# Performance work log

Measured on AMD Instinct MI355X. Metric: run time of the kernel, lower is better.

## Reference

```python
import jax, jax.numpy as jnp
import numpy as np

T, B, D_IN, H = 512, 256, 512, 128

def setup_inputs() -> dict:
    key = jax.random.key(0)
    ks = jax.random.split(key, 6)
    c0 = jax.random.normal(ks[0], (B, H), jnp.float32)
    h0 = jax.random.normal(ks[1], (B, H), jnp.float32)
    obs = jax.random.normal(ks[2], (T, B, D_IN), jnp.float32)
    done = jax.random.randint(ks[3], (T, B), 0, 2).astype(jnp.bool_)
    Wi = jax.random.normal(ks[4], (D_IN, 4 * H), jnp.float32) * (1.0 / np.sqrt(D_IN))
    Wh = jax.random.normal(ks[5], (H, 4 * H), jnp.float32) * (1.0 / np.sqrt(H))
    b = jnp.zeros((4 * H,), jnp.float32)
    return {"c0": c0, "h0": h0, "obs": obs, "done": done, "Wi": Wi, "Wh": Wh, "b": b}

def reference(c0, h0, obs, done, Wi, Wh, b):
    # Time-scanned flax LSTMCell with done-masked state reset.
    # Carry reset: where(done, initialize_carry()=zeros, old_state).
    # Flax LSTMCell gates (order i,f,g,o): sigmoid/sigmoid/tanh/sigmoid,
    # dense_i has no bias, dense_h has bias b.
    def step(carry, inp):
        c, h = carry
        x, d = inp                      # x: [B, D_IN], d: [B]
        keep = jnp.logical_not(d)[:, None]
        c = jnp.where(keep, c, 0.0)
        h = jnp.where(keep, h, 0.0)
        gates = x @ Wi + h @ Wh + b     # [B, 4H]
        i, f, g, o = jnp.split(gates, 4, axis=-1)
        new_c = jax.nn.sigmoid(f) * c + jax.nn.sigmoid(i) * jnp.tanh(g)
        new_h = jax.nn.sigmoid(o) * jnp.tanh(new_c)
        return (new_c, new_h), new_h

    (cT, hT), ys = jax.lax.scan(step, (c0, h0), (obs, done))
    return ys, cT, hT
```

## Files before the change

### kernel.cpp

```cpp
#include <hip/hip_runtime.h>
#include <hip/hip_bf16.h>
#include <cstdint>
#include <cstddef>

#define TT  512
#define BB  256
#define DIN 512
#define HH  128
#define NG  512

typedef __bf16 bf16x8 __attribute__((ext_vector_type(8)));
typedef float  f32x4  __attribute__((ext_vector_type(4)));

__device__ __forceinline__ float fast_sig(float x) {
  float e = __builtin_amdgcn_exp2f(-1.44269504f * x);
  return __builtin_amdgcn_rcpf(1.f + e);
}
__device__ __forceinline__ float fast_tanh(float x) {
  float e = __builtin_amdgcn_exp2f(-2.88539008f * x);
  return __builtin_fmaf(2.f, __builtin_amdgcn_rcpf(1.f + e), -1.f);
}

__device__ __forceinline__ void lgkm_barrier() {
  asm volatile("s_waitcnt lgkmcnt(0)\n\ts_barrier" ::: "memory");
}

__device__ __forceinline__ int ld_flag(const int* p) {
  return __hip_atomic_load(p, __ATOMIC_RELAXED, __HIP_MEMORY_SCOPE_AGENT);
}
__device__ __forceinline__ uint2 ld_xg8(const __bf16* p) {
  unsigned long long v = __hip_atomic_load((const unsigned long long*)p,
                                           __ATOMIC_RELAXED, __HIP_MEMORY_SCOPE_AGENT);
  union { unsigned long long u; uint2 v2; } cv; cv.u = v;
  return cv.v2;
}

__global__ void wconv_kernel(const float* __restrict__ Wi, const float* __restrict__ Wh,
                             __bf16* __restrict__ WiT, __bf16* __restrict__ WhT,
                             int* __restrict__ flags) {
  int idx = blockIdx.x * 256 + threadIdx.x;
  if (blockIdx.x == 0) {
    flags[threadIdx.x] = 0;
    flags[threadIdx.x + 256] = 0;
  }
  if (idx < DIN * NG) {
    int n = idx >> 9, k = idx & 511;
    WiT[(size_t)n * DIN + k] = (__bf16)Wi[(size_t)k * NG + n];
  }
  if (idx < HH * NG) {
    int n = idx >> 7, k = idx & 127;
    WhT[(size_t)n * HH + k] = (__bf16)Wh[(size_t)k * NG + n];
  }
}

__device__ __forceinline__ void gemm_body(
    const float* __restrict__ obs, const __bf16* __restrict__ WiT,
    const float* __restrict__ bias, __bf16* __restrict__ Xg,
    int* __restrict__ flags, int bid, __bf16 (*Alds)[40]) {
  const int tid  = threadIdx.x;
  const int wave = tid >> 6, lane = tid & 63;
  const int l15  = lane & 15, q = lane >> 4;
  const size_t m0 = (size_t)bid * 128;

  const f32x4 fzero = {0.f, 0.f, 0.f, 0.f};
  f32x4 acc[8][4];
#pragma unroll
  for (int i = 0; i < 8; i++)
#pragma unroll
    for (int jj = 0; jj < 4; jj++) acc[i][jj] = fzero;

  const int am = tid >> 2, aq = tid & 3;
  const float* aptr = obs + (m0 + am) * DIN + aq * 8;
  const __bf16* bptr[4];
#pragma unroll
  for (int nt = 0; nt < 4; nt++)
    bptr[nt] = WiT + (size_t)(wave * 64 + nt * 16 + l15) * DIN + q * 8;

  float4 a0[2], a1[2];
  bf16x8 bs[2][4];
  a0[0] = *(const float4*)(aptr);      a1[0] = *(const float4*)(aptr + 4);
  a0[1] = *(const float4*)(aptr + 32); a1[1] = *(const float4*)(aptr + 36);
#pragma unroll
  for (int nt = 0; nt < 4; nt++) {
    bs[0][nt] = *(const bf16x8*)(bptr[nt]);
    bs[1][nt] = *(const bf16x8*)(bptr[nt] + 32);
  }

#pragma unroll
  for (int kc = 0; kc < DIN; kc += 32) {
    const int sl = (kc >> 5) & 1;
    if (kc) lgkm_barrier();
    {
      float4 f0 = a0[sl], f1 = a1[sl];
      bf16x8 v = {(__bf16)f0.x, (__bf16)f0.y, (__bf16)f0.z, (__bf16)f0.w,
                  (__bf16)f1.x, (__bf16)f1.y, (__bf16)f1.z, (__bf16)f1.w};
      *(bf16x8*)&Alds[am][aq * 8] = v;
    }
    lgkm_barrier();
    int kp = kc + 64; if (kp > DIN - 32) kp = DIN - 32;
    a0[sl] = *(const float4*)(aptr + kp);
    a1[sl] = *(const float4*)(aptr + kp + 4);
#pragma unroll
    for (int mt = 0; mt < 8; mt++) {
      bf16x8 af = *(const bf16x8*)&Alds[mt * 16 + l15][q * 8];
#pragma unroll
      for (int nt = 0; nt < 4; nt++)
        acc[mt][nt] = __builtin_amdgcn_mfma_f32_16x16x32_bf16(af, bs[sl][nt], acc[mt][nt], 0, 0, 0);
    }
#pragma unroll
    for (int nt = 0; nt < 4; nt++)
      bs[sl][nt] = *(const bf16x8*)(bptr[nt] + kp);
  }

  const int t = bid >> 1;
  const int half = bid & 1;
#pragma unroll
  for (int mt = 0; mt < 8; mt++) {
    const int bg = half * 8 + mt;
#pragma unroll
    for (int nt = 0; nt < 4; nt++) {
      const int n = wave * 64 + nt * 16 + l15;
      const int g = n >> 7, jj = n & 127;
      const float bb = bias[n];
      __bf16* base = Xg + (size_t)(t * 16 + bg) * 4 * 2048 + jj * 16 + q * 4 + g;
#pragma unroll
      for (int r = 0; r < 4; r++)
        base[(size_t)r * 2048] = (__bf16)(acc[mt][nt][r] + bb);
    }
  }

  __syncthreads();
  if (tid == 0) {
    __threadfence();
    __hip_atomic_fetch_add(flags + t, 1, __ATOMIC_RELEASE, __HIP_MEMORY_SCOPE_AGENT);
  }
}

template<int R0>
__device__ __forceinline__ void scan_body(
    const __bf16* __restrict__ Xg, const __bf16* __restrict__ WhT,
    const int* __restrict__ done, const float* __restrict__ c0,
    const float* __restrict__ h0, float* __restrict__ out,
    const int* __restrict__ flags,
    int bg, __bf16 (*hlds)[16][HH + 8]) {
  const int tid  = threadIdx.x;
  const int wave = tid >> 6, lane = tid & 63;
  const int l15  = lane & 15, q = lane >> 4;
  const int b0 = bg * 16;
  const int j  = wave * 16 + l15;
  const int b  = b0 + q * 4 + R0;
  const int row = q * 4 + R0;

  bf16x8 bfrag[4][4];
#pragma unroll
  for (int g = 0; g < 4; g++)
#pragma unroll
    for (int ks = 0; ks < 4; ks++)
      bfrag[g][ks] = *(const bf16x8*)(WhT + (size_t)(g * HH + j) * HH + ks * 32 + q * 8);

  for (int i = tid; i < 2 * 16 * (HH + 8); i += 512) ((__bf16*)hlds)[i] = (__bf16)0.f;
  __syncthreads();
  const int d0 = done[b];
  float c = c0[(size_t)b * HH + j];
  hlds[0][row][j] = d0 ? (__bf16)0.f : (__bf16)h0[(size_t)b * HH + j];
  __syncthreads();

  const size_t tstride = (size_t)16 * 4 * 2048;
  const __bf16* xpA = Xg + (size_t)(bg * 4 + R0) * 2048 + j * 16 + q * 4;
  const __bf16* xpB = xpA + tstride;
  const int* dpA = done + b;
  const int* dpB = dpA + BB;

  { int f = ld_flag(flags + 0); while (f < 2) f = ld_flag(flags + 0); }
  { int f = ld_flag(flags + 1); while (f < 2) f = ld_flag(flags + 1); }
  uint2 xgA = ld_xg8(xpA);  xpA += 2 * tstride;
  uint2 xgB = ld_xg8(xpB);  xpB += 2 * tstride;
  int dnA = *dpA; dpA += 2 * BB;
  int dnB = *dpB; dpB += 2 * BB;
  int fA = ld_flag(flags + 2);
  int fB = ld_flag(flags + 3);

  float* op = out + (size_t)b * HH + j;
  float nh = 0.f;

#define SCAN_STEP(XGC, DNC, DNW, RD, WR)                                      \
  {                                                                           \
    bf16x8 af[4];                                                             \
    _Pragma("unroll")                                                         \
    for (int ks = 0; ks < 4; ks++)                                            \
      af[ks] = *(const bf16x8*)&hlds[RD][l15][ks * 32 + q * 8];               \
    union { uint2 u; __bf16 h[4]; } ux; ux.u = (XGC);                         \
    float gv[4];                                                              \
    _Pragma("unroll")                                                         \
    for (int g = 0; g < 4; g++) {                                             \
      float xv = (float)ux.h[g];                                              \
      f32x4 accA = {xv, xv, xv, xv};                                          \
      accA = __builtin_amdgcn_mfma_f32_16x16x32_bf16(af[0], bfrag[g][0], accA, 0, 0, 0); \
      accA = __builtin_amdgcn_mfma_f32_16x16x32_bf16(af[2], bfrag[g][2], accA, 0, 0, 0); \
      f32x4 accB = {0.f, 0.f, 0.f, 0.f};                                      \
      accB = __builtin_amdgcn_mfma_f32_16x16x32_bf16(af[1], bfrag[g][1], accB, 0, 0, 0); \
      accB = __builtin_amdgcn_mfma_f32_16x16x32_bf16(af[3], bfrag[g][3], accB, 0, 0, 0); \
      gv[g] = accA[R0] + accB[R0];                                            \
    }                                                                         \
    float cprev = (DNC) ? 0.f : c;                                            \
    float nc = __builtin_fmaf(fast_sig(gv[1]), cprev, fast_sig(gv[0]) * fast_tanh(gv[2])); \
    nh = fast_sig(gv[3]) * fast_tanh(nc);                                     \
    c = nc;                                                                   \
    hlds[WR][row][j] = (DNW) ? (__bf16)0.f : (__bf16)nh;                      \
    *op = nh; op += BB * HH;                                                  \
    lgkm_barrier();                                                           \
  }

  for (int t = 0; t < TT; t += 2) {
    {
      uint2 xg_c = xgA; int dn_c = dnA, dn_w = dnB;
      if (t + 2 < TT) {
        while (fA < 2) fA = ld_flag(flags + t + 2);
        xgA = ld_xg8(xpA); dnA = *dpA;
        fA = (t + 4 < TT) ? ld_flag(flags + t + 4) : 2;
      }
      xpA += 2 * tstride; dpA += 2 * BB;
      SCAN_STEP(xg_c, dn_c, dn_w, 0, 1)
    }
    {
      uint2 xg_c = xgB; int dn_c = dnB, dn_w = dnA;
      if (t + 3 < TT) {
        while (fB < 2) fB = ld_flag(flags + t + 3);
        xgB = ld_xg8(xpB); dnB = *dpB;
        fB = (t + 5 < TT) ? ld_flag(flags + t + 5) : 2;
      }
      xpB += 2 * tstride; dpB += 2 * BB;
      SCAN_STEP(xg_c, dn_c, dn_w, 1, 0)
    }
  }
#undef SCAN_STEP

  float* cT = out + (size_t)TT * BB * HH;
  float* hT = cT + (size_t)BB * HH;
  cT[(size_t)b * HH + j] = c;
  hT[(size_t)b * HH + j] = nh;
}

__global__ __launch_bounds__(512, 2)
void fused_kernel(const float* __restrict__ obs, const __bf16* __restrict__ WiT,
                  const float* __restrict__ bias, __bf16* __restrict__ Xg,
                  const __bf16* __restrict__ WhT, const int* __restrict__ done,
                  const float* __restrict__ c0, const float* __restrict__ h0,
                  float* __restrict__ out, int* __restrict__ flags) {
  __shared__ __align__(16) char smem[10240];
  if (blockIdx.x < 64) {
    __bf16 (*hlds)[16][HH + 8] = (__bf16 (*)[16][HH + 8])smem;
    const int bg = blockIdx.x >> 2;
    switch (blockIdx.x & 3) {
      case 0: scan_body<0>(Xg, WhT, done, c0, h0, out, flags, bg, hlds); break;
      case 1: scan_body<1>(Xg, WhT, done, c0, h0, out, flags, bg, hlds); break;
      case 2: scan_body<2>(Xg, WhT, done, c0, h0, out, flags, bg, hlds); break;
      case 3: scan_body<3>(Xg, WhT, done, c0, h0, out, flags, bg, hlds); break;
    }
  } else {
    gemm_body(obs, WiT, bias, Xg, flags, blockIdx.x - 64, (__bf16 (*)[40])smem);
  }
}

extern "C" void kernel_launch(void* const* d_in, const int* in_sizes, int n_in,
                              void* d_out, int out_size, void* d_ws, size_t ws_size,
                              hipStream_t stream) {
  const float* c0   = (const float*)d_in[0];
  const float* h0   = (const float*)d_in[1];
  const float* obs  = (const float*)d_in[2];
  const int*   done = (const int*)d_in[3];
  const float* Wi   = (const float*)d_in[4];
  const float* Wh   = (const float*)d_in[5];
  const float* bias = (const float*)d_in[6];
  float* out = (float*)d_out;

  char* ws = (char*)d_ws;
  __bf16* Xg  = (__bf16*)ws;
  __bf16* WiT = (__bf16*)(ws + (size_t)134217728);
  __bf16* WhT = (__bf16*)(ws + (size_t)134217728 + 524288);
  int*  flags = (int*)(ws + (size_t)134217728 + 524288 + 131072);

  wconv_kernel<<<dim3(1024), dim3(256), 0, stream>>>(Wi, Wh, WiT, WhT, flags);
  fused_kernel<<<dim3(1088), dim3(512), 0, stream>>>(obs, WiT, bias, Xg, WhT, done,
                                                     c0, h0, out, flags);
}
```

Baseline: 774.1 us.

## Restage GEMM epilogue through LDS, pad flags, and add sleep in spin-waits

The GEMM producer blocks now load the A operand straight from global memory into MFMA fragments and drop the LDS double-buffer and its barriers. The epilogue stages each tile in LDS and writes it to Xg as coalesced agent-scope 64-bit stores. Flags are padded to one per 64 bytes to avoid false sharing, the producer drops its threadfence and uses a relaxed increment, and the scan spin-waits gain s_sleep to cut polling traffic. In exchange, A reuse across waves moves from LDS to cache, and the weaker release ordering could let consumers read stale Xg data.

```diff
diff --git a/kernel.cpp b/kernel.cpp
--- a/kernel.cpp
+++ b/kernel.cpp
@@ -34,15 +34,17 @@
   union { unsigned long long u; uint2 v2; } cv; cv.u = v;
   return cv.v2;
 }
+__device__ __forceinline__ void st_agent_u64(unsigned long long* p, unsigned long long v) {
+  __hip_atomic_store(p, v, __ATOMIC_RELAXED, __HIP_MEMORY_SCOPE_AGENT);
+}
+
+#define FLAG(t) ((t) * 16)
 
 __global__ void wconv_kernel(const float* __restrict__ Wi, const float* __restrict__ Wh,
                              __bf16* __restrict__ WiT, __bf16* __restrict__ WhT,
                              int* __restrict__ flags) {
   int idx = blockIdx.x * 256 + threadIdx.x;
-  if (blockIdx.x == 0) {
-    flags[threadIdx.x] = 0;
-    flags[threadIdx.x + 256] = 0;
-  }
+  if (idx < TT * 16) flags[idx] = 0;
   if (idx < DIN * NG) {
     int n = idx >> 9, k = idx & 511;
     WiT[(size_t)n * DIN + k] = (__bf16)Wi[(size_t)k * NG + n];
@@ -56,7 +58,7 @@
 __device__ __forceinline__ void gemm_body(
     const float* __restrict__ obs, const __bf16* __restrict__ WiT,
     const float* __restrict__ bias, __bf16* __restrict__ Xg,
-    int* __restrict__ flags, int bid, __bf16 (*Alds)[40]) {
+    int* __restrict__ flags, int bid, __bf16* eld ) {
   const int tid  = threadIdx.x;
   const int wave = tid >> 6, lane = tid & 63;
   const int l15  = lane & 15, q = lane >> 4;
@@ -69,71 +71,58 @@
 #pragma unroll
     for (int jj = 0; jj < 4; jj++) acc[i][jj] = fzero;
 
-  const int am = tid >> 2, aq = tid & 3;
-  const float* aptr = obs + (m0 + am) * DIN + aq * 8;
+  const float* aptr0 = obs + (m0 + l15) * DIN + q * 8;
   const __bf16* bptr[4];
 #pragma unroll
   for (int nt = 0; nt < 4; nt++)
     bptr[nt] = WiT + (size_t)(wave * 64 + nt * 16 + l15) * DIN + q * 8;
 
-  float4 a0[2], a1[2];
-  bf16x8 bs[2][4];
-  a0[0] = *(const float4*)(aptr);      a1[0] = *(const float4*)(aptr + 4);
-  a0[1] = *(const float4*)(aptr + 32); a1[1] = *(const float4*)(aptr + 36);
-#pragma unroll
-  for (int nt = 0; nt < 4; nt++) {
-    bs[0][nt] = *(const bf16x8*)(bptr[nt]);
-    bs[1][nt] = *(const bf16x8*)(bptr[nt] + 32);
-  }
-
-#pragma unroll
+#pragma unroll 2
   for (int kc = 0; kc < DIN; kc += 32) {
-    const int sl = (kc >> 5) & 1;
-    if (kc) lgkm_barrier();
-    {
-      float4 f0 = a0[sl], f1 = a1[sl];
-      bf16x8 v = {(__bf16)f0.x, (__bf16)f0.y, (__bf16)f0.z, (__bf16)f0.w,
-                  (__bf16)f1.x, (__bf16)f1.y, (__bf16)f1.z, (__bf16)f1.w};
-      *(bf16x8*)&Alds[am][aq * 8] = v;
-    }
-    lgkm_barrier();
-    int kp = kc + 64; if (kp > DIN - 32) kp = DIN - 32;
-    a0[sl] = *(const float4*)(aptr + kp);
-    a1[sl] = *(const float4*)(aptr + kp + 4);
+    bf16x8 bfr[4];
+#pragma unroll
+    for (int nt = 0; nt < 4; nt++)
+      bfr[nt] = *(const bf16x8*)(bptr[nt] + kc);
 #pragma unroll
     for (int mt = 0; mt < 8; mt++) {
-      bf16x8 af = *(const bf16x8*)&Alds[mt * 16 + l15][q * 8];
+      const float* ap = aptr0 + (size_t)mt * 16 * DIN + kc;
+      float4 f0 = *(const float4*)(ap);
+      float4 f1 = *(const float4*)(ap + 4);
+      bf16x8 af = {(__bf16)f0.x, (__bf16)f0.y, (__bf16)f0.z, (__bf16)f0.w,
+                   (__bf16)f1.x, (__bf16)f1.y, (__bf16)f1.z, (__bf16)f1.w};
 #pragma unroll
       for (int nt = 0; nt < 4; nt++)
-        acc[mt][nt] = __builtin_amdgcn_mfma_f32_16x16x32_bf16(af, bs[sl][nt], acc[mt][nt], 0, 0, 0);
-    }
-#pragma unroll
-    for (int nt = 0; nt < 4; nt++)
-      bs[sl][nt] = *(const bf16x8*)(bptr[nt] + kp);
+        acc[mt][nt] = __builtin_amdgcn_mfma_f32_16x16x32_bf16(af, bfr[nt], acc[mt][nt], 0, 0, 0);
+    }
   }
 
   const int t = bid >> 1;
   const int half = bid & 1;
-#pragma unroll
+#pragma unroll 1
   for (int mt = 0; mt < 8; mt++) {
-    const int bg = half * 8 + mt;
+    __syncthreads();
 #pragma unroll
     for (int nt = 0; nt < 4; nt++) {
       const int n = wave * 64 + nt * 16 + l15;
       const int g = n >> 7, jj = n & 127;
       const float bb = bias[n];
-      __bf16* base = Xg + (size_t)(t * 16 + bg) * 4 * 2048 + jj * 16 + q * 4 + g;
 #pragma unroll
       for (int r = 0; r < 4; r++)
-        base[(size_t)r * 2048] = (__bf16)(acc[mt][nt][r] + bb);
-    }
+        eld[r * 2048 + jj * 16 + q * 4 + g] = (__bf16)(acc[mt][nt][r] + bb);
+    }
+    __syncthreads();
+    const int bg = half * 8 + mt;
+    unsigned long long* dst =
+        (unsigned long long*)(Xg + (size_t)(t * 16 + bg) * 8192);
+    const unsigned long long* src = (const unsigned long long*)eld;
+#pragma unroll
+    for (int u = 0; u < 4; u++)
+      st_agent_u64(dst + tid * 4 + u, src[tid * 4 + u]);
   }
 
   __syncthreads();
-  if (tid == 0) {
-    __threadfence();
-    __hip_atomic_fetch_add(flags + t, 1, __ATOMIC_RELEASE, __HIP_MEMORY_SCOPE_AGENT);
-  }
+  if (tid == 0)
+    __hip_atomic_fetch_add(flags + FLAG(t), 1, __ATOMIC_RELAXED, __HIP_MEMORY_SCOPE_AGENT);
 }
 
 template<int R0>
@@ -171,14 +160,16 @@
   const int* dpA = done + b;
   const int* dpB = dpA + BB;
 
-  { int f = ld_flag(flags + 0); while (f < 2) f = ld_flag(flags + 0); }
-  { int f = ld_flag(flags + 1); while (f < 2) f = ld_flag(flags + 1); }
+  { int f = ld_flag(flags + FLAG(0));
+    while (f < 2) { __builtin_amdgcn_s_sleep(2); f = ld_flag(flags + FLAG(0)); } }
+  { int f = ld_flag(flags + FLAG(1));
+    while (f < 2) { __builtin_amdgcn_s_sleep(2); f = ld_flag(flags + FLAG(1)); } }
   uint2 xgA = ld_xg8(xpA);  xpA += 2 * tstride;
   uint2 xgB = ld_xg8(xpB);  xpB += 2 * tstride;
   int dnA = *dpA; dpA += 2 * BB;
   int dnB = *dpB; dpB += 2 * BB;
-  int fA = ld_flag(flags + 2);
-  int fB = ld_flag(flags + 3);
+  int fA = ld_flag(flags + FLAG(2));
+  int fB = ld_flag(flags + FLAG(3));
 
   float* op = out + (size_t)b * HH + j;
   float nh = 0.f;
@@ -215,9 +206,9 @@
     {
       uint2 xg_c = xgA; int dn_c = dnA, dn_w = dnB;
       if (t + 2 < TT) {
-        while (fA < 2) fA = ld_flag(flags + t + 2);
+        while (fA < 2) { __builtin_amdgcn_s_sleep(1); fA = ld_flag(flags + FLAG(t + 2)); }
         xgA = ld_xg8(xpA); dnA = *dpA;
-        fA = (t + 4 < TT) ? ld_flag(flags + t + 4) : 2;
+        fA = (t + 4 < TT) ? ld_flag(flags + FLAG(t + 4)) : 2;
       }
       xpA += 2 * tstride; dpA += 2 * BB;
       SCAN_STEP(xg_c, dn_c, dn_w, 0, 1)
@@ -225,9 +216,9 @@
     {
       uint2 xg_c = xgB; int dn_c = dnB, dn_w = dnA;
       if (t + 3 < TT) {
-        while (fB < 2) fB = ld_flag(flags + t + 3);
+        while (fB < 2) { __builtin_amdgcn_s_sleep(1); fB = ld_flag(flags + FLAG(t + 3)); }
         xgB = ld_xg8(xpB); dnB = *dpB;
-        fB = (t + 5 < TT) ? ld_flag(flags + t + 5) : 2;
+        fB = (t + 5 < TT) ? ld_flag(flags + FLAG(t + 5)) : 2;
       }
       xpB += 2 * tstride; dpB += 2 * BB;
       SCAN_STEP(xg_c, dn_c, dn_w, 1, 0)
@@ -247,7 +238,7 @@
                   const __bf16* __restrict__ WhT, const int* __restrict__ done,
                   const float* __restrict__ c0, const float* __restrict__ h0,
                   float* __restrict__ out, int* __restrict__ flags) {
-  __shared__ __align__(16) char smem[10240];
+  __shared__ __align__(16) char smem[16384];
   if (blockIdx.x < 64) {
     __bf16 (*hlds)[16][HH + 8] = (__bf16 (*)[16][HH + 8])smem;
     const int bg = blockIdx.x >> 2;
@@ -258,7 +249,7 @@
       case 3: scan_body<3>(Xg, WhT, done, c0, h0, out, flags, bg, hlds); break;
     }
   } else {
-    gemm_body(obs, WiT, bias, Xg, flags, blockIdx.x - 64, (__bf16 (*)[40])smem);
+    gemm_body(obs, WiT, bias, Xg, flags, blockIdx.x - 64, (__bf16*)smem);
   }
 }
 
```

Result: slower. 1.172 ms (+51.4%).

## Make GEMM blocks persistent, pad readiness flags, and add sleep to spin-waits

Applied to the files above, without the earlier changes.

The fused launch shrinks from 1088 blocks to 256. Each GEMM block now loops over tiles with stride 192, so all blocks stay resident alongside the scan blocks. Readiness flags are spaced 16 ints apart so each sits on its own cache line, which avoids false sharing between producers and pollers. Spin-waits now call s_sleep to cut polling pressure on memory. The risks are that 192 persistent GEMM blocks may produce Xg more slowly than the scan consumes it, and that sleeping adds wake-up latency on the critical recurrent path.

```diff
diff --git a/kernel.cpp b/kernel.cpp
--- a/kernel.cpp
+++ b/kernel.cpp
@@ -35,14 +35,13 @@
   return cv.v2;
 }
 
+#define FLAG(t) ((t) * 16)
+
 __global__ void wconv_kernel(const float* __restrict__ Wi, const float* __restrict__ Wh,
                              __bf16* __restrict__ WiT, __bf16* __restrict__ WhT,
                              int* __restrict__ flags) {
   int idx = blockIdx.x * 256 + threadIdx.x;
-  if (blockIdx.x == 0) {
-    flags[threadIdx.x] = 0;
-    flags[threadIdx.x + 256] = 0;
-  }
+  if (idx < TT * 16) flags[idx] = 0;
   if (idx < DIN * NG) {
     int n = idx >> 9, k = idx & 511;
     WiT[(size_t)n * DIN + k] = (__bf16)Wi[(size_t)k * NG + n];
@@ -56,83 +55,85 @@
 __device__ __forceinline__ void gemm_body(
     const float* __restrict__ obs, const __bf16* __restrict__ WiT,
     const float* __restrict__ bias, __bf16* __restrict__ Xg,
-    int* __restrict__ flags, int bid, __bf16 (*Alds)[40]) {
+    int* __restrict__ flags, int p, __bf16 (*Alds)[40]) {
   const int tid  = threadIdx.x;
   const int wave = tid >> 6, lane = tid & 63;
   const int l15  = lane & 15, q = lane >> 4;
-  const size_t m0 = (size_t)bid * 128;
-
-  const f32x4 fzero = {0.f, 0.f, 0.f, 0.f};
-  f32x4 acc[8][4];
-#pragma unroll
-  for (int i = 0; i < 8; i++)
-#pragma unroll
-    for (int jj = 0; jj < 4; jj++) acc[i][jj] = fzero;
-
   const int am = tid >> 2, aq = tid & 3;
-  const float* aptr = obs + (m0 + am) * DIN + aq * 8;
+
   const __bf16* bptr[4];
 #pragma unroll
   for (int nt = 0; nt < 4; nt++)
     bptr[nt] = WiT + (size_t)(wave * 64 + nt * 16 + l15) * DIN + q * 8;
 
-  float4 a0[2], a1[2];
-  bf16x8 bs[2][4];
-  a0[0] = *(const float4*)(aptr);      a1[0] = *(const float4*)(aptr + 4);
-  a0[1] = *(const float4*)(aptr + 32); a1[1] = *(const float4*)(aptr + 36);
-#pragma unroll
-  for (int nt = 0; nt < 4; nt++) {
-    bs[0][nt] = *(const bf16x8*)(bptr[nt]);
-    bs[1][nt] = *(const bf16x8*)(bptr[nt] + 32);
-  }
-
-#pragma unroll
-  for (int kc = 0; kc < DIN; kc += 32) {
-    const int sl = (kc >> 5) & 1;
-    if (kc) lgkm_barrier();
-    {
-      float4 f0 = a0[sl], f1 = a1[sl];
-      bf16x8 v = {(__bf16)f0.x, (__bf16)f0.y, (__bf16)f0.z, (__bf16)f0.w,
-                  (__bf16)f1.x, (__bf16)f1.y, (__bf16)f1.z, (__bf16)f1.w};
-      *(bf16x8*)&Alds[am][aq * 8] = v;
-    }
-    lgkm_barrier();
-    int kp = kc + 64; if (kp > DIN - 32) kp = DIN - 32;
-    a0[sl] = *(const float4*)(aptr + kp);
-    a1[sl] = *(const float4*)(aptr + kp + 4);
+  for (int bid = p; bid < 2 * TT; bid += 192) {
+    const size_t m0 = (size_t)bid * 128;
+
+    const f32x4 fzero = {0.f, 0.f, 0.f, 0.f};
+    f32x4 acc[8][4];
+#pragma unroll
+    for (int i = 0; i < 8; i++)
+#pragma unroll
+      for (int jj = 0; jj < 4; jj++) acc[i][jj] = fzero;
+
+    const float* aptr = obs + (m0 + am) * DIN + aq * 8;
+
+    float4 a0[2], a1[2];
+    bf16x8 bs[2][4];
+    a0[0] = *(const float4*)(aptr);      a1[0] = *(const float4*)(aptr + 4);
+    a0[1] = *(const float4*)(aptr + 32); a1[1] = *(const float4*)(aptr + 36);
+#pragma unroll
+    for (int nt = 0; nt < 4; nt++) {
+      bs[0][nt] = *(const bf16x8*)(bptr[nt]);
+      bs[1][nt] = *(const bf16x8*)(bptr[nt] + 32);
+    }
+
+#pragma unroll
+    for (int kc = 0; kc < DIN; kc += 32) {
+      const int sl = (kc >> 5) & 1;
+      if (kc) lgkm_barrier();
+      {
+        float4 f0 = a0[sl], f1 = a1[sl];
+        bf16x8 v = {(__bf16)f0.x, (__bf16)f0.y, (__bf16)f0.z, (__bf16)f0.w,
+                    (__bf16)f1.x, (__bf16)f1.y, (__bf16)f1.z, (__bf16)f1.w};
+        *(bf16x8*)&Alds[am][aq * 8] = v;
+      }
+      lgkm_barrier();
+      int kp = kc + 64; if (kp > DIN - 32) kp = DIN - 32;
+      a0[sl] = *(const float4*)(aptr + kp);
+      a1[sl] = *(const float4*)(aptr + kp + 4);
+#pragma unroll
+      for (int mt = 0; mt < 8; mt++) {
+        bf16x8 af = *(const bf16x8*)&Alds[mt * 16 + l15][q * 8];
+#pragma unroll
+        for (int nt = 0; nt < 4; nt++)
+          acc[mt][nt] = __builtin_amdgcn_mfma_f32_16x16x32_bf16(af, bs[sl][nt], acc[mt][nt], 0, 0, 0);
+      }
+#pragma unroll
+      for (int nt = 0; nt < 4; nt++)
+        bs[sl][nt] = *(const bf16x8*)(bptr[nt] + kp);
+    }
+
+    const int t = bid >> 1;
+    const int half = bid & 1;
 #pragma unroll
     for (int mt = 0; mt < 8; mt++) {
-      bf16x8 af = *(const bf16x8*)&Alds[mt * 16 + l15][q * 8];
-#pragma unroll
-      for (int nt = 0; nt < 4; nt++)
-        acc[mt][nt] = __builtin_amdgcn_mfma_f32_16x16x32_bf16(af, bs[sl][nt], acc[mt][nt], 0, 0, 0);
-    }
-#pragma unroll
-    for (int nt = 0; nt < 4; nt++)
-      bs[sl][nt] = *(const bf16x8*)(bptr[nt] + kp);
-  }
-
-  const int t = bid >> 1;
-  const int half = bid & 1;
-#pragma unroll
-  for (int mt = 0; mt < 8; mt++) {
-    const int bg = half * 8 + mt;
-#pragma unroll
-    for (int nt = 0; nt < 4; nt++) {
-      const int n = wave * 64 + nt * 16 + l15;
-      const int g = n >> 7, jj = n & 127;
-      const float bb = bias[n];
-      __bf16* base = Xg + (size_t)(t * 16 + bg) * 4 * 2048 + jj * 16 + q * 4 + g;
-#pragma unroll
-      for (int r = 0; r < 4; r++)
-        base[(size_t)r * 2048] = (__bf16)(acc[mt][nt][r] + bb);
-    }
-  }
-
-  __syncthreads();
-  if (tid == 0) {
-    __threadfence();
-    __hip_atomic_fetch_add(flags + t, 1, __ATOMIC_RELEASE, __HIP_MEMORY_SCOPE_AGENT);
+      const int bg = half * 8 + mt;
+#pragma unroll
+      for (int nt = 0; nt < 4; nt++) {
+        const int n = wave * 64 + nt * 16 + l15;
+        const int g = n >> 7, jj = n & 127;
+        const float bb = bias[n];
+        __bf16* base = Xg + (size_t)(t * 16 + bg) * 4 * 2048 + jj * 16 + q * 4 + g;
+#pragma unroll
+        for (int r = 0; r < 4; r++)
+          base[(size_t)r * 2048] = (__bf16)(acc[mt][nt][r] + bb);
+      }
+    }
+
+    __syncthreads();
+    if (tid == 0)
+      __hip_atomic_fetch_add(flags + FLAG(t), 1, __ATOMIC_RELEASE, __HIP_MEMORY_SCOPE_AGENT);
   }
 }
 
@@ -171,14 +172,16 @@
   const int* dpA = done + b;
   const int* dpB = dpA + BB;
 
-  { int f = ld_flag(flags + 0); while (f < 2) f = ld_flag(flags + 0); }
-  { int f = ld_flag(flags + 1); while (f < 2) f = ld_flag(flags + 1); }
+  { int f = ld_flag(flags + FLAG(0));
+    while (f < 2) { __builtin_amdgcn_s_sleep(2); f = ld_flag(flags + FLAG(0)); } }
+  { int f = ld_flag(flags + FLAG(1));
+    while (f < 2) { __builtin_amdgcn_s_sleep(2); f = ld_flag(flags + FLAG(1)); } }
   uint2 xgA = ld_xg8(xpA);  xpA += 2 * tstride;
   uint2 xgB = ld_xg8(xpB);  xpB += 2 * tstride;
   int dnA = *dpA; dpA += 2 * BB;
   int dnB = *dpB; dpB += 2 * BB;
-  int fA = ld_flag(flags + 2);
-  int fB = ld_flag(flags + 3);
+  int fA = ld_flag(flags + FLAG(2));
+  int fB = ld_flag(flags + FLAG(3));
 
   float* op = out + (size_t)b * HH + j;
   float nh = 0.f;
@@ -215,9 +218,9 @@
     {
       uint2 xg_c = xgA; int dn_c = dnA, dn_w = dnB;
       if (t + 2 < TT) {
-        while (fA < 2) fA = ld_flag(flags + t + 2);
+        while (fA < 2) { __builtin_amdgcn_s_sleep(1); fA = ld_flag(flags + FLAG(t + 2)); }
         xgA = ld_xg8(xpA); dnA = *dpA;
-        fA = (t + 4 < TT) ? ld_flag(flags + t + 4) : 2;
+        fA = (t + 4 < TT) ? ld_flag(flags + FLAG(t + 4)) : 2;
       }
       xpA += 2 * tstride; dpA += 2 * BB;
       SCAN_STEP(xg_c, dn_c, dn_w, 0, 1)
@@ -225,9 +228,9 @@
     {
       uint2 xg_c = xgB; int dn_c = dnB, dn_w = dnA;
       if (t + 3 < TT) {
-        while (fB < 2) fB = ld_flag(flags + t + 3);
+        while (fB < 2) { __builtin_amdgcn_s_sleep(1); fB = ld_flag(flags + FLAG(t + 3)); }
         xgB = ld_xg8(xpB); dnB = *dpB;
-        fB = (t + 5 < TT) ? ld_flag(flags + t + 5) : 2;
+        fB = (t + 5 < TT) ? ld_flag(flags + FLAG(t + 5)) : 2;
       }
       xpB += 2 * tstride; dpB += 2 * BB;
       SCAN_STEP(xg_c, dn_c, dn_w, 1, 0)
@@ -281,6 +284,6 @@
   int*  flags = (int*)(ws + (size_t)134217728 + 524288 + 131072);
 
   wconv_kernel<<<dim3(1024), dim3(256), 0, stream>>>(Wi, Wh, WiT, WhT, flags);
-  fused_kernel<<<dim3(1088), dim3(512), 0, stream>>>(obs, WiT, bias, Xg, WhT, done,
-                                                     c0, h0, out, flags);
-}
+  fused_kernel<<<dim3(256), dim3(512), 0, stream>>>(obs, WiT, bias, Xg, WhT, done,
+                                                    c0, h0, out, flags);
+}
```

New measurement: 762.5 us. About the same (-1.5%).
